# Performance work log

Measured on AMD Instinct MI355X. Metric: run time of the kernel, lower is better.

Reference implementation:

```python
import jax, jax.numpy as jnp
import numpy as np

NC = 100000   # output rows of the sparse matrix
NT = 100000   # input columns of the sparse matrix
NNZ = 640000  # number of nonzeros (COO entries)
D = 128       # dense feature width


def setup_inputs() -> dict:
    key = jax.random.key(0)
    k1, k2, k3 = jax.random.split(key, 3)
    mat = jax.random.normal(k1, (NT, D), dtype=jnp.float32)
    row = jax.random.randint(k2, (NNZ,), 0, NC, dtype=jnp.int32)
    col = jax.random.randint(k3, (NNZ,), 0, NT, dtype=jnp.int32)
    return {"mat": mat, "row": row, "col": col}


def reference(mat, row, col):
    # Sparse binary (Nc x Nt) @ dense (Nt x D):
    # out[r] += mat[c] for each nonzero (r, c).
    # The TF original batches gather + tensor_scatter_nd_add over the
    # index list; a single gather + segment_sum computes the same result.
    vals = jnp.take(mat, col, axis=0)                      # [nnz, D]
    out = jax.ops.segment_sum(vals, row, num_segments=NC)  # [Nc, D]
    return out
```

## Files before the change

### kernel.cpp

```cpp
#include <hip/hip_runtime.h>


#define NC_CONST 100000
#define NNZ_CONST 640000
#define D_CONST 128
#define OVF_MAX 65536
#define SCAN_BLK 256
#define NBLK ((NC_CONST + SCAN_BLK - 1) / SCAN_BLK)

typedef float v4f __attribute__((ext_vector_type(4)));

template <int CAP>
__global__ __launch_bounds__(256) void place_bucket_kernel(
    const int* __restrict__ row, const int* __restrict__ col,
    int* __restrict__ cnt, int* __restrict__ ovf_cnt,
    int* __restrict__ ovf, int* __restrict__ bucket) {
    int i = blockIdx.x * blockDim.x + threadIdx.x;
    if (i >= NNZ_CONST) return;
    int r = row[i];
    int c = col[i];
    int idx = atomicAdd(&cnt[r], 1);
    if (idx < CAP) {
        bucket[r * CAP + idx] = c;
    } else {
        int o = atomicAdd(ovf_cnt, 1);
        if (o < OVF_MAX) { ovf[2 * o] = r; ovf[2 * o + 1] = c; }
    }
}

template <int CAP>
__global__ __launch_bounds__(256) void segsum_bucket_kernel(
    const float* __restrict__ mat, const int* __restrict__ cnt,
    const int* __restrict__ ovf_cnt, const int* __restrict__ ovf,
    const int* __restrict__ bucket, float* __restrict__ out) {
    int g = blockIdx.x * 8 + (threadIdx.x >> 5);
    int lane = threadIdx.x & 31;
    if (g >= NC_CONST) return;

    int n = cnt[g];
    if (n > CAP) n = CAP;

    int myc = (lane < n) ? bucket[g * CAP + lane] : 0;

    float ax = 0.f, ay = 0.f, az = 0.f, aw = 0.f;
    for (int j = 0; j < n; ++j) {
        int c = __shfl(myc, j, 32);
        const float4 v =
            reinterpret_cast<const float4*>(mat + (size_t)c * D_CONST)[lane];
        ax += v.x; ay += v.y; az += v.z; aw += v.w;
    }

    int novf = *ovf_cnt;
    if (novf > OVF_MAX) novf = OVF_MAX;
    for (int o = 0; o < novf; ++o) {
        if (ovf[2 * o] == g) {
            int c = ovf[2 * o + 1];
            const float4 v =
                reinterpret_cast<const float4*>(mat + (size_t)c * D_CONST)[lane];
            ax += v.x; ay += v.y; az += v.z; aw += v.w;
        }
    }

    v4f r;
    r.x = ax; r.y = ay; r.z = az; r.w = aw;
    __builtin_nontemporal_store(
        r, reinterpret_cast<v4f*>(out + (size_t)g * D_CONST) + lane);
}

__global__ __launch_bounds__(256) void hist_kernel(
    const int* __restrict__ row, int* __restrict__ cnt) {
    int i = blockIdx.x * blockDim.x + threadIdx.x;
    if (i < NNZ_CONST) atomicAdd(&cnt[row[i]], 1);
}

__global__ __launch_bounds__(SCAN_BLK) void scan_reduce_kernel(
    const int* __restrict__ cnt, int* __restrict__ blocksums) {
    __shared__ int lds[SCAN_BLK];
    int i = blockIdx.x * SCAN_BLK + threadIdx.x;
    int v = (i < NC_CONST) ? cnt[i] : 0;
    lds[threadIdx.x] = v;
    __syncthreads();
    for (int s = SCAN_BLK / 2; s > 0; s >>= 1) {
        if (threadIdx.x < s) lds[threadIdx.x] += lds[threadIdx.x + s];
        __syncthreads();
    }
    if (threadIdx.x == 0) blocksums[blockIdx.x] = lds[0];
}

__global__ __launch_bounds__(512) void scan_spine_kernel(
    const int* __restrict__ blocksums, int* __restrict__ blockoffs) {
    __shared__ int lds[512];
    int t = threadIdx.x;
    int v = (t < NBLK) ? blocksums[t] : 0;
    lds[t] = v;
    __syncthreads();
    for (int s = 1; s < 512; s <<= 1) {
        int add = (t >= s) ? lds[t - s] : 0;
        __syncthreads();
        lds[t] += add;
        __syncthreads();
    }
    if (t < NBLK) blockoffs[t] = lds[t] - v;
}

__global__ __launch_bounds__(SCAN_BLK) void scan_final_kernel(
    const int* __restrict__ cnt, const int* __restrict__ blockoffs,
    int* __restrict__ offs, int* __restrict__ cursor) {
    __shared__ int lds[SCAN_BLK];
    int i = blockIdx.x * SCAN_BLK + threadIdx.x;
    int t = threadIdx.x;
    int v = (i < NC_CONST) ? cnt[i] : 0;
    lds[t] = v;
    __syncthreads();
    for (int s = 1; s < SCAN_BLK; s <<= 1) {
        int add = (t >= s) ? lds[t - s] : 0;
        __syncthreads();
        lds[t] += add;
        __syncthreads();
    }
    int off = blockoffs[blockIdx.x] + lds[t] - v;
    if (i < NC_CONST) {
        offs[i] = off;
        cursor[i] = off;
        if (i == NC_CONST - 1) offs[NC_CONST] = off + v;
    }
}

__global__ __launch_bounds__(256) void place_kernel(
    const int* __restrict__ row, const int* __restrict__ col,
    int* __restrict__ cursor, int* __restrict__ sorted_col) {
    int i = blockIdx.x * blockDim.x + threadIdx.x;
    if (i < NNZ_CONST) {
        int p = atomicAdd(&cursor[row[i]], 1);
        sorted_col[p] = col[i];
    }
}

__global__ __launch_bounds__(256) void segsum_kernel(
    const float* __restrict__ mat, const int* __restrict__ offs,
    const int* __restrict__ sorted_col, float* __restrict__ out) {
    int g = blockIdx.x * 8 + (threadIdx.x >> 5);
    int lane = threadIdx.x & 31;
    if (g >= NC_CONST) return;
    int beg = offs[g];
    int end = offs[g + 1];
    float ax = 0.f, ay = 0.f, az = 0.f, aw = 0.f;
    for (int j = beg; j < end; ++j) {
        int c = sorted_col[j];
        const float4 v =
            reinterpret_cast<const float4*>(mat + (size_t)c * D_CONST)[lane];
        ax += v.x; ay += v.y; az += v.z; aw += v.w;
    }
    float4 r; r.x = ax; r.y = ay; r.z = az; r.w = aw;
    reinterpret_cast<float4*>(out + (size_t)g * D_CONST)[lane] = r;
}

__global__ __launch_bounds__(256) void scatter_add_kernel(
    const float* __restrict__ mat, const int* __restrict__ row,
    const int* __restrict__ col, float* __restrict__ out) {
    int gid = blockIdx.x * blockDim.x + threadIdx.x;
    int nz = gid >> 5;
    int lane = gid & 31;
    if (nz >= NNZ_CONST) return;
    int r = row[nz];
    int c = col[nz];
    const float4 v =
        reinterpret_cast<const float4*>(mat + (size_t)c * D_CONST)[lane];
    float* o = out + (size_t)r * D_CONST + (size_t)lane * 4;
    atomicAdd(o + 0, v.x);
    atomicAdd(o + 1, v.y);
    atomicAdd(o + 2, v.z);
    atomicAdd(o + 3, v.w);
}

template <int CAP>
static void launch_bucket_path(const float* mat, const int* row, const int* col,
                               float* out, void* d_ws, hipStream_t stream) {
    int* cnt     = (int*)d_ws;
    int* ovf_cnt = cnt + NC_CONST;
    int* ovf     = ovf_cnt + 1;
    int* bucket  = ovf + 2 * OVF_MAX;

    (void)hipMemsetAsync(cnt, 0, (size_t)(NC_CONST + 1) * sizeof(int), stream);

    place_bucket_kernel<CAP><<<(NNZ_CONST + 255) / 256, 256, 0, stream>>>(
        row, col, cnt, ovf_cnt, ovf, bucket);
    segsum_bucket_kernel<CAP><<<(NC_CONST + 7) / 8, 256, 0, stream>>>(
        mat, cnt, ovf_cnt, ovf, bucket, out);
}

extern "C" void kernel_launch(void* const* d_in, const int* in_sizes, int n_in,
                              void* d_out, int out_size, void* d_ws, size_t ws_size,
                              hipStream_t stream) {
    const float* mat = (const float*)d_in[0];
    const int* row   = (const int*)d_in[1];
    const int* col   = (const int*)d_in[2];
    float* out = (float*)d_out;

    const size_t need32 =
        (size_t)(NC_CONST + 1 + 2 * OVF_MAX + (size_t)NC_CONST * 32) * sizeof(int);
    const size_t need16 =
        (size_t)(NC_CONST + 1 + 2 * OVF_MAX + (size_t)NC_CONST * 16) * sizeof(int);
    const size_t need_sort =
        (size_t)(NC_CONST + NC_CONST + 1 + NC_CONST + NNZ_CONST + 2 * NBLK) *
        sizeof(int);

    if (ws_size >= need32) {
        launch_bucket_path<32>(mat, row, col, out, d_ws, stream);
    } else if (ws_size >= need16) {
        launch_bucket_path<16>(mat, row, col, out, d_ws, stream);
    } else if (ws_size >= need_sort) {
        int* cnt        = (int*)d_ws;
        int* offs       = cnt + NC_CONST;
        int* cursor     = offs + NC_CONST + 1;
        int* sorted_col = cursor + NC_CONST;
        int* blocksums  = sorted_col + NNZ_CONST;
        int* blockoffs  = blocksums + NBLK;

        (void)hipMemsetAsync(cnt, 0, (size_t)NC_CONST * sizeof(int), stream);
        hist_kernel<<<(NNZ_CONST + 255) / 256, 256, 0, stream>>>(row, cnt);
        scan_reduce_kernel<<<NBLK, SCAN_BLK, 0, stream>>>(cnt, blocksums);
        scan_spine_kernel<<<1, 512, 0, stream>>>(blocksums, blockoffs);
        scan_final_kernel<<<NBLK, SCAN_BLK, 0, stream>>>(cnt, blockoffs, offs, cursor);
        place_kernel<<<(NNZ_CONST + 255) / 256, 256, 0, stream>>>(row, col, cursor, sorted_col);
        segsum_kernel<<<(NC_CONST + 7) / 8, 256, 0, stream>>>(mat, offs, sorted_col, out);
    } else {
        (void)hipMemsetAsync(out, 0, (size_t)out_size * sizeof(float), stream);
        const long long total = (long long)NNZ_CONST * 32;
        scatter_add_kernel<<<(int)((total + 255) / 256), 256, 0, stream>>>(
            mat, row, col, out);
    }
}
```

Baseline: 180.7 us.

## Partition bucket placement and segment sum by XCD-local row ranges

Blocks are assigned to XCDs by blockIdx modulo 8, and each XCD handles only rows in its own contiguous range for both the placement and the segment-sum kernels. The aim is to keep atomics on cnt and the bucket writes inside one XCD's L2, avoiding cross-die coherence traffic. In exchange, every XCD group scans the full row array, so row reads go up eightfold. The scheme also depends on the hardware's round-robin block-to-XCD mapping.

```diff
diff --git a/kernel.cpp b/kernel.cpp
--- a/kernel.cpp
+++ b/kernel.cpp
@@ -5,42 +5,55 @@
 #define NNZ_CONST 640000
 #define D_CONST 128
 #define OVF_MAX 65536
+#define NXCD 8
+#define RANGE 12500
+#define PLACE_BLOCKS 1024
 #define SCAN_BLK 256
 #define NBLK ((NC_CONST + SCAN_BLK - 1) / SCAN_BLK)
 
 typedef float v4f __attribute__((ext_vector_type(4)));
 
 template <int CAP>
-__global__ __launch_bounds__(256) void place_bucket_kernel(
+__global__ __launch_bounds__(256) void place_xcd_kernel(
     const int* __restrict__ row, const int* __restrict__ col,
     int* __restrict__ cnt, int* __restrict__ ovf_cnt,
     int* __restrict__ ovf, int* __restrict__ bucket) {
-    int i = blockIdx.x * blockDim.x + threadIdx.x;
-    if (i >= NNZ_CONST) return;
-    int r = row[i];
-    int c = col[i];
-    int idx = atomicAdd(&cnt[r], 1);
-    if (idx < CAP) {
-        bucket[r * CAP + idx] = c;
-    } else {
-        int o = atomicAdd(ovf_cnt, 1);
-        if (o < OVF_MAX) { ovf[2 * o] = r; ovf[2 * o + 1] = c; }
+    const int xcd = blockIdx.x % NXCD;
+    const int gidx = blockIdx.x / NXCD;
+    const int lo = xcd * RANGE;
+    const int hi = lo + RANGE;
+    const int nthreads = (PLACE_BLOCKS / NXCD) * 256;
+
+    for (int i = gidx * 256 + threadIdx.x; i < NNZ_CONST; i += nthreads) {
+        int r = row[i];
+        if (r >= lo && r < hi) {
+            int c = col[i];
+            int idx = atomicAdd(&cnt[r], 1);
+            if (idx < CAP) {
+                bucket[(size_t)r * CAP + idx] = c;
+            } else {
+                int o = atomicAdd(ovf_cnt, 1);
+                if (o < OVF_MAX) { ovf[2 * o] = r; ovf[2 * o + 1] = c; }
+            }
+        }
     }
 }
 
 template <int CAP>
-__global__ __launch_bounds__(256) void segsum_bucket_kernel(
+__global__ __launch_bounds__(256) void segsum_xcd_kernel(
     const float* __restrict__ mat, const int* __restrict__ cnt,
     const int* __restrict__ ovf_cnt, const int* __restrict__ ovf,
     const int* __restrict__ bucket, float* __restrict__ out) {
-    int g = blockIdx.x * 8 + (threadIdx.x >> 5);
+    const int xcd = blockIdx.x % NXCD;
+    const int local = blockIdx.x / NXCD;
+    int g = xcd * RANGE + local * 8 + (threadIdx.x >> 5);
     int lane = threadIdx.x & 31;
-    if (g >= NC_CONST) return;
+    if (g >= xcd * RANGE + RANGE) return;
 
     int n = cnt[g];
     if (n > CAP) n = CAP;
 
-    int myc = (lane < n) ? bucket[g * CAP + lane] : 0;
+    int myc = (lane < n) ? bucket[(size_t)g * CAP + lane] : 0;
 
     float ax = 0.f, ay = 0.f, az = 0.f, aw = 0.f;
     for (int j = 0; j < n; ++j) {
@@ -183,9 +196,11 @@
 
     (void)hipMemsetAsync(cnt, 0, (size_t)(NC_CONST + 1) * sizeof(int), stream);
 
-    place_bucket_kernel<CAP><<<(NNZ_CONST + 255) / 256, 256, 0, stream>>>(
+    place_xcd_kernel<CAP><<<PLACE_BLOCKS, 256, 0, stream>>>(
         row, col, cnt, ovf_cnt, ovf, bucket);
-    segsum_bucket_kernel<CAP><<<(NC_CONST + 7) / 8, 256, 0, stream>>>(
+
+    const int seg_blocks = ((RANGE + 7) / 8) * NXCD;
+    segsum_xcd_kernel<CAP><<<seg_blocks, 256, 0, stream>>>(
         mat, cnt, ovf_cnt, ovf, bucket, out);
 }
 
```

New measurement: 171.5 us. -5.1%, faster.
